# Performance work log

Hardware: AMD Instinct MI355X
Metric: run time of the kernel (lower is better)

Reference implementation:

```python
import jax, jax.numpy as jnp
import numpy as np

E = 128      # embedding_dim
H = 64       # hidden_dim
B = 2048     # batch
L = 200      # history length
NEG = -1e30  # stand-in for -inf (avoids NaN for all-pad rows; same math when any key unmasked)


def setup_inputs() -> dict:
    key = jax.random.key(0)
    ks = jax.random.split(key, 10)
    s1 = 1.0 / np.sqrt(4 * E)
    s2 = 1.0 / np.sqrt(H)
    return {
        "query": jax.random.normal(ks[0], (B, E), jnp.float32),
        "keys": jax.random.normal(ks[1], (B, L, E), jnp.float32),
        "mask": jax.random.randint(ks[2], (B, L), 0, 2, jnp.int32),
        "W1": jax.random.uniform(ks[3], (4 * E, H), jnp.float32, -s1, s1),
        "b1": jax.random.uniform(ks[4], (H,), jnp.float32, -s1, s1),
        "W2": jax.random.uniform(ks[5], (H, H), jnp.float32, -s2, s2),
        "b2": jax.random.uniform(ks[6], (H,), jnp.float32, -s2, s2),
        "W3": jax.random.uniform(ks[7], (H, 1), jnp.float32, -s2, s2),
        "b3": jax.random.uniform(ks[8], (1,), jnp.float32, -s2, s2),
        "no_hist": jax.random.normal(ks[9], (E,), jnp.float32) * 0.001,
    }


def reference(query, keys, mask, W1, b1, W2, b2, W3, b3, no_hist):
    # q expanded over L, 4-way concat features: [q, k, q*k, q-k] -> (B, L, 4E)
    q = jnp.broadcast_to(query[:, None, :], keys.shape)
    attn_in = jnp.concatenate([q, keys, q * keys, q - keys], axis=-1)
    # 3-layer MLP scorer -> (B, L)
    h = jax.nn.relu(attn_in @ W1 + b1)
    h = jax.nn.relu(h @ W2 + b2)
    scores = (h @ W3 + b3)[..., 0]
    # masked softmax over L, then zero masked slots and renormalize
    m = mask.astype(scores.dtype)
    scores = jnp.where(m == 0, NEG, scores)
    attn = jax.nn.softmax(scores, axis=1) * m
    denom = jnp.sum(attn, axis=1, keepdims=True)
    attn = attn / (denom + 1e-12)
    # weighted sum of keys -> (B, E)
    user_interest = jnp.einsum("bl,ble->be", attn, keys)
    # rows with no history get the learned no-hist embedding
    all_pad = jnp.sum(m, axis=1) == 0  # (B,)
    user_interest = jnp.where(all_pad[:, None], no_hist[None, :], user_interest)
    return user_interest
```

## Files before the change

### kernel.cpp

```cpp
#include <hip/hip_runtime.h>


#define NB 2048
#define LE 128
#define LH 64
#define LL 200

typedef short bf16x8 __attribute__((ext_vector_type(8)));
typedef float f32x4 __attribute__((ext_vector_type(4)));

__device__ float g_BD[8192];
__device__ float g_Cq[8192];
__device__ float g_AD[8192];
__device__ short g_W2T[4096];

__device__ __forceinline__ short f2bf(float f) {
  unsigned u = __float_as_uint(f);
  u += 0x7fffu + ((u >> 16) & 1u);
  return (short)(u >> 16);
}

__global__ void k0_prep(const float* __restrict__ W1, const float* __restrict__ W2) {
  int idx = blockIdx.x * 256 + threadIdx.x;
  if (idx < 8192) {
    int h = idx >> 7, e = idx & 127;
    g_BD[idx] = W1[(128 + e) * LH + h] - W1[(384 + e) * LH + h];
    g_Cq[idx] = W1[(256 + e) * LH + h];
    int e2 = idx >> 6, h2 = idx & 63;
    g_AD[idx] = W1[e2 * LH + h2] + W1[(384 + e2) * LH + h2];
    if (idx < 4096) {
      int c = idx >> 6, k = idx & 63;
      g_W2T[idx] = f2bf(W2[k * LH + c]);
    }
  }
}

struct __align__(16) SM {
  short flds1[16 * 64 * 8];
  short flds2[8 * 64 * 8];
  short h1[4][16 * 72];
  float scores[208];
  float q[128];
  float bias1[64];
  float b2s[64];
  float w3s[64];
  float red[16];
};

__global__ void __launch_bounds__(256, 4)
din_attn(const float* __restrict__ query, const float* __restrict__ keysg,
         const int* __restrict__ mask, const float* __restrict__ b1,
         const float* __restrict__ b2, const float* __restrict__ W3,
         const float* __restrict__ no_hist, float* __restrict__ out)
{
  __shared__ SM sm;
  const int b    = blockIdx.x;
  const int t    = threadIdx.x;
  const int lane = t & 63;
  const int wv   = t >> 6;
  const int col  = lane & 15;
  const int quad = lane >> 4;

  int my_mask = 0;
  if (t < LL) my_mask = mask[b * LL + t];
  if (t < LE) sm.q[t] = query[b * LE + t];
  if (t < LH) { sm.b2s[t] = b2[t]; sm.w3s[t] = W3[t]; }
  __syncthreads();

  #pragma unroll
  for (int i = 0; i < 4; ++i) {
    int idx = (t + 256 * i) * 8;
    int h = idx >> 7, e0 = idx & 127;
    float4 bd0 = *(const float4*)&g_BD[idx];
    float4 bd1 = *(const float4*)&g_BD[idx + 4];
    float4 c0  = *(const float4*)&g_Cq[idx];
    float4 c1  = *(const float4*)&g_Cq[idx + 4];
    bf16x8 w;
    w[0] = f2bf(bd0.x + sm.q[e0 + 0] * c0.x);
    w[1] = f2bf(bd0.y + sm.q[e0 + 1] * c0.y);
    w[2] = f2bf(bd0.z + sm.q[e0 + 2] * c0.z);
    w[3] = f2bf(bd0.w + sm.q[e0 + 3] * c0.w);
    w[4] = f2bf(bd1.x + sm.q[e0 + 4] * c1.x);
    w[5] = f2bf(bd1.y + sm.q[e0 + 5] * c1.y);
    w[6] = f2bf(bd1.z + sm.q[e0 + 6] * c1.z);
    w[7] = f2bf(bd1.w + sm.q[e0 + 7] * c1.w);
    int n = h >> 4, cc = h & 15, kt = e0 >> 5, qd = (e0 >> 3) & 3;
    *(bf16x8*)&sm.flds1[(((n * 4 + kt) * 64) + qd * 16 + cc) * 8] = w;
  }
  {
    int l = t & 63, f0 = t >> 6;
    #pragma unroll
    for (int ii = 0; ii < 2; ++ii) {
      int f = f0 + ii * 4;
      int n = f >> 1, k2 = f & 1;
      int cc = l & 15, qd = l >> 4;
      *(bf16x8*)&sm.flds2[(f * 64 + l) * 8] =
          *(const bf16x8*)&g_W2T[(n * 16 + cc) * 64 + k2 * 32 + qd * 8];
    }
  }
  {
    int h = lane;
    float acc = 0.f;
    #pragma unroll 8
    for (int e = wv * 32; e < wv * 32 + 32; ++e)
      acc = fmaf(sm.q[e], g_AD[e * LH + h], acc);
    float* biasp = (float*)&sm.h1[0][0];
    biasp[wv * 64 + h] = acc;
  }
  __syncthreads();

  if (t < LH) {
    const float* biasp = (const float*)&sm.h1[0][0];
    sm.bias1[t] = b1[t] + biasp[t] + biasp[64 + t] + biasp[128 + t] + biasp[192 + t];
  }
  __syncthreads();

  const float* kb = keysg + (size_t)b * LL * LE;
  short* h1w = &sm.h1[wv][0];
  const int mts[4] = {wv, wv + 4, wv + 8, 12};
  bf16x8 ka[4][4];

  auto load_tile = [&](bf16x8 (&a)[4], int mt) {
    int row = mt * 16 + col;
    row = row < LL ? row : LL - 1;
    const float* rp = kb + row * LE;
    #pragma unroll
    for (int kt = 0; kt < 4; ++kt) {
      float4 v0 = *(const float4*)&rp[kt * 32 + quad * 8];
      float4 v1 = *(const float4*)&rp[kt * 32 + quad * 8 + 4];
      bf16x8 av;
      av[0] = f2bf(v0.x); av[1] = f2bf(v0.y); av[2] = f2bf(v0.z); av[3] = f2bf(v0.w);
      av[4] = f2bf(v1.x); av[5] = f2bf(v1.y); av[6] = f2bf(v1.z); av[7] = f2bf(v1.w);
      a[kt] = av;
    }
  };

  auto compute_tile = [&](const bf16x8 (&a)[4], int mt) {
    #pragma unroll
    for (int n = 0; n < 4; ++n) {
      f32x4 acc = {0.f, 0.f, 0.f, 0.f};
      #pragma unroll
      for (int kt = 0; kt < 4; ++kt) {
        bf16x8 wf = *(const bf16x8*)&sm.flds1[((n * 4 + kt) * 64 + lane) * 8];
        acc = __builtin_amdgcn_mfma_f32_16x16x32_bf16(a[kt], wf, acc, 0, 0, 0);
      }
      float bias = sm.bias1[n * 16 + col];
      #pragma unroll
      for (int j = 0; j < 4; ++j)
        h1w[(quad * 4 + j) * 72 + n * 16 + col] = f2bf(fmaxf(acc[j] + bias, 0.f));
    }
    bf16x8 a2[2];
    #pragma unroll
    for (int k2 = 0; k2 < 2; ++k2)
      a2[k2] = *(const bf16x8*)&h1w[col * 72 + k2 * 32 + quad * 8];
    float p[4] = {0.f, 0.f, 0.f, 0.f};
    #pragma unroll
    for (int n = 0; n < 4; ++n) {
      bf16x8 w20 = *(const bf16x8*)&sm.flds2[((n * 2 + 0) * 64 + lane) * 8];
      bf16x8 w21 = *(const bf16x8*)&sm.flds2[((n * 2 + 1) * 64 + lane) * 8];
      f32x4 c2 = {0.f, 0.f, 0.f, 0.f};
      c2 = __builtin_amdgcn_mfma_f32_16x16x32_bf16(a2[0], w20, c2, 0, 0, 0);
      c2 = __builtin_amdgcn_mfma_f32_16x16x32_bf16(a2[1], w21, c2, 0, 0, 0);
      float bb = sm.b2s[n * 16 + col];
      float w3 = sm.w3s[n * 16 + col];
      #pragma unroll
      for (int j = 0; j < 4; ++j)
        p[j] = fmaf(fmaxf(c2[j] + bb, 0.f), w3, p[j]);
    }
    #pragma unroll
    for (int j = 0; j < 4; ++j) {
      #pragma unroll
      for (int off = 1; off < 16; off <<= 1)
        p[j] += __shfl_xor(p[j], off);
      if (col == 0) sm.scores[mt * 16 + quad * 4 + j] = p[j];
    }
  };

  load_tile(ka[0], mts[0]);
  load_tile(ka[1], mts[1]);
  compute_tile(ka[0], mts[0]);
  load_tile(ka[2], mts[2]);
  compute_tile(ka[1], mts[1]);
  if (wv == 0) load_tile(ka[3], 12);
  compute_tile(ka[2], mts[2]);
  if (wv == 0) compute_tile(ka[3], 12);
  __syncthreads();

  float sc = (t < LL) ? sm.scores[t] : -3.0e38f;
  float vmax = (my_mask != 0) ? sc : -3.0e38f;
  #pragma unroll
  for (int off = 1; off < 64; off <<= 1) vmax = fmaxf(vmax, __shfl_xor(vmax, off));
  if (lane == 0) sm.red[wv] = vmax;
  __syncthreads();
  float M = fmaxf(fmaxf(sm.red[0], sm.red[1]), fmaxf(sm.red[2], sm.red[3]));
  float ex = (t < LL && my_mask != 0) ? __expf(sc - M) : 0.f;
  float vsum = ex;
  #pragma unroll
  for (int off = 1; off < 64; off <<= 1) vsum += __shfl_xor(vsum, off);
  if (lane == 0) sm.red[4 + wv] = vsum;
  __syncthreads();
  float Z = sm.red[4] + sm.red[5] + sm.red[6] + sm.red[7];
  bool allpad = !(Z > 0.f);
  float rz = allpad ? 0.f : (1.f / Z);
  if (t < 208) sm.scores[t] = (t < LL) ? ex * rz : 0.f;
  __syncthreads();

  {
    const int nt = (wv == 0) ? 4 : 3;
    float aw[4] = {0.f, 0.f, 0.f, 0.f};
    #pragma unroll
    for (int i = 0; i < 4; ++i)
      if (i < nt) aw[i] = sm.scores[mts[i] * 16 + col];

    float* redf = (float*)&sm.h1[0][0];
    #pragma unroll
    for (int kt = 0; kt < 4; ++kt) {
      float s[8] = {0.f, 0.f, 0.f, 0.f, 0.f, 0.f, 0.f, 0.f};
      #pragma unroll
      for (int i = 0; i < 4; ++i) {
        if (i < nt) {
          const int* kv = (const int*)&ka[i][kt];
          #pragma unroll
          for (int w = 0; w < 4; ++w) {
            unsigned u = (unsigned)kv[w];
            s[2 * w]     = fmaf(aw[i], __uint_as_float(u << 16), s[2 * w]);
            s[2 * w + 1] = fmaf(aw[i], __uint_as_float(u & 0xffff0000u), s[2 * w + 1]);
          }
        }
      }
      #pragma unroll
      for (int j = 0; j < 8; ++j) {
        #pragma unroll
        for (int off = 1; off < 16; off <<= 1)
          s[j] += __shfl_xor(s[j], off);
      }
      if (col == 0) {
        #pragma unroll
        for (int j = 0; j < 8; ++j)
          redf[wv * 128 + kt * 32 + quad * 8 + j] = s[j];
      }
    }
    __syncthreads();
    if (t < LE) {
      float s = redf[t] + redf[128 + t] + redf[256 + t] + redf[384 + t];
      if (allpad) s = no_hist[t];
      out[b * LE + t] = s;
    }
  }
}

extern "C" void kernel_launch(void* const* d_in, const int* in_sizes, int n_in,
                              void* d_out, int out_size, void* d_ws, size_t ws_size,
                              hipStream_t stream) {
  (void)in_sizes; (void)n_in; (void)ws_size; (void)out_size; (void)d_ws;
  const float* query   = (const float*)d_in[0];
  const float* keysg   = (const float*)d_in[1];
  const int*   mask    = (const int*)d_in[2];
  const float* W1      = (const float*)d_in[3];
  const float* b1      = (const float*)d_in[4];
  const float* W2      = (const float*)d_in[5];
  const float* b2      = (const float*)d_in[6];
  const float* W3      = (const float*)d_in[7];
  const float* no_hist = (const float*)d_in[9];

  k0_prep<<<32, 256, 0, stream>>>(W1, W2);
  din_attn<<<NB, 256, 0, stream>>>(query, keysg, mask, b1, b2, W3, no_hist,
                                   (float*)d_out);
}
```

Measured before the change: 319.6 us.

## Use packed bf16 conversion, transposed MFMA output, and butterfly shuffle reductions

```diff
diff --git a/kernel.cpp b/kernel.cpp
--- a/kernel.cpp
+++ b/kernel.cpp
@@ -18,6 +18,12 @@
   unsigned u = __float_as_uint(f);
   u += 0x7fffu + ((u >> 16) & 1u);
   return (short)(u >> 16);
+}
+
+__device__ __forceinline__ unsigned cvtpk(float a, float b) {
+  unsigned d;
+  asm("v_cvt_pk_bf16_f32 %0, %1, %2" : "=v"(d) : "v"(a), "v"(b));
+  return d;
 }
 
 __global__ void k0_prep(const float* __restrict__ W1, const float* __restrict__ W2) {
@@ -38,13 +44,14 @@
 struct __align__(16) SM {
   short flds1[16 * 64 * 8];
   short flds2[8 * 64 * 8];
-  short h1[4][16 * 72];
+  short h1[4][16 * 68];
   float scores[208];
   float q[128];
   float bias1[64];
   float b2s[64];
   float w3s[64];
   float red[16];
+  float redf[512];
 };
 
 __global__ void __launch_bounds__(256, 4)
@@ -75,17 +82,13 @@
     float4 bd1 = *(const float4*)&g_BD[idx + 4];
     float4 c0  = *(const float4*)&g_Cq[idx];
     float4 c1  = *(const float4*)&g_Cq[idx + 4];
-    bf16x8 w;
-    w[0] = f2bf(bd0.x + sm.q[e0 + 0] * c0.x);
-    w[1] = f2bf(bd0.y + sm.q[e0 + 1] * c0.y);
-    w[2] = f2bf(bd0.z + sm.q[e0 + 2] * c0.z);
-    w[3] = f2bf(bd0.w + sm.q[e0 + 3] * c0.w);
-    w[4] = f2bf(bd1.x + sm.q[e0 + 4] * c1.x);
-    w[5] = f2bf(bd1.y + sm.q[e0 + 5] * c1.y);
-    w[6] = f2bf(bd1.z + sm.q[e0 + 6] * c1.z);
-    w[7] = f2bf(bd1.w + sm.q[e0 + 7] * c1.w);
+    int4 w;
+    w.x = (int)cvtpk(bd0.x + sm.q[e0 + 0] * c0.x, bd0.y + sm.q[e0 + 1] * c0.y);
+    w.y = (int)cvtpk(bd0.z + sm.q[e0 + 2] * c0.z, bd0.w + sm.q[e0 + 3] * c0.w);
+    w.z = (int)cvtpk(bd1.x + sm.q[e0 + 4] * c1.x, bd1.y + sm.q[e0 + 5] * c1.y);
+    w.w = (int)cvtpk(bd1.z + sm.q[e0 + 6] * c1.z, bd1.w + sm.q[e0 + 7] * c1.w);
     int n = h >> 4, cc = h & 15, kt = e0 >> 5, qd = (e0 >> 3) & 3;
-    *(bf16x8*)&sm.flds1[(((n * 4 + kt) * 64) + qd * 16 + cc) * 8] = w;
+    *(int4*)&sm.flds1[(((n * 4 + kt) * 64) + qd * 16 + cc) * 8] = w;
   }
   {
     int l = t & 63, f0 = t >> 6;
@@ -128,10 +131,12 @@
     for (int kt = 0; kt < 4; ++kt) {
       float4 v0 = *(const float4*)&rp[kt * 32 + quad * 8];
       float4 v1 = *(const float4*)&rp[kt * 32 + quad * 8 + 4];
-      bf16x8 av;
-      av[0] = f2bf(v0.x); av[1] = f2bf(v0.y); av[2] = f2bf(v0.z); av[3] = f2bf(v0.w);
-      av[4] = f2bf(v1.x); av[5] = f2bf(v1.y); av[6] = f2bf(v1.z); av[7] = f2bf(v1.w);
-      a[kt] = av;
+      int4 w;
+      w.x = (int)cvtpk(v0.x, v0.y);
+      w.y = (int)cvtpk(v0.z, v0.w);
+      w.z = (int)cvtpk(v1.x, v1.y);
+      w.w = (int)cvtpk(v1.z, v1.w);
+      a[kt] = *(bf16x8*)&w;
     }
   };
 
@@ -142,17 +147,18 @@
       #pragma unroll
       for (int kt = 0; kt < 4; ++kt) {
         bf16x8 wf = *(const bf16x8*)&sm.flds1[((n * 4 + kt) * 64 + lane) * 8];
-        acc = __builtin_amdgcn_mfma_f32_16x16x32_bf16(a[kt], wf, acc, 0, 0, 0);
+        acc = __builtin_amdgcn_mfma_f32_16x16x32_bf16(wf, a[kt], acc, 0, 0, 0);
       }
-      float bias = sm.bias1[n * 16 + col];
-      #pragma unroll
-      for (int j = 0; j < 4; ++j)
-        h1w[(quad * 4 + j) * 72 + n * 16 + col] = f2bf(fmaxf(acc[j] + bias, 0.f));
+      float4 bb = *(const float4*)&sm.bias1[n * 16 + quad * 4];
+      int2 wr;
+      wr.x = (int)cvtpk(fmaxf(acc[0] + bb.x, 0.f), fmaxf(acc[1] + bb.y, 0.f));
+      wr.y = (int)cvtpk(fmaxf(acc[2] + bb.z, 0.f), fmaxf(acc[3] + bb.w, 0.f));
+      *(int2*)&h1w[col * 68 + n * 16 + quad * 4] = wr;
     }
     bf16x8 a2[2];
     #pragma unroll
     for (int k2 = 0; k2 < 2; ++k2)
-      a2[k2] = *(const bf16x8*)&h1w[col * 72 + k2 * 32 + quad * 8];
+      a2[k2] = *(const bf16x8*)&h1w[col * 68 + k2 * 32 + quad * 8];
     float p[4] = {0.f, 0.f, 0.f, 0.f};
     #pragma unroll
     for (int n = 0; n < 4; ++n) {
@@ -167,12 +173,18 @@
       for (int j = 0; j < 4; ++j)
         p[j] = fmaf(fmaxf(c2[j] + bb, 0.f), w3, p[j]);
     }
-    #pragma unroll
-    for (int j = 0; j < 4; ++j) {
-      #pragma unroll
-      for (int off = 1; off < 16; off <<= 1)
-        p[j] += __shfl_xor(p[j], off);
-      if (col == 0) sm.scores[mt * 16 + quad * 4 + j] = p[j];
+    {
+      bool s8 = (col & 8) != 0;
+      float k0 = s8 ? p[2] : p[0], d0 = s8 ? p[0] : p[2];
+      float k1 = s8 ? p[3] : p[1], d1 = s8 ? p[1] : p[3];
+      k0 += __shfl_xor(d0, 8);
+      k1 += __shfl_xor(d1, 8);
+      bool s4 = (col & 4) != 0;
+      float u = s4 ? k1 : k0, du = s4 ? k0 : k1;
+      u += __shfl_xor(du, 4);
+      u += __shfl_xor(u, 2);
+      u += __shfl_xor(u, 1);
+      if ((col & 3) == 0) sm.scores[mt * 16 + quad * 4 + (col >> 2)] = u;
     }
   };
 
@@ -207,42 +219,44 @@
 
   {
     const int nt = (wv == 0) ? 4 : 3;
-    float aw[4] = {0.f, 0.f, 0.f, 0.f};
-    #pragma unroll
-    for (int i = 0; i < 4; ++i)
-      if (i < nt) aw[i] = sm.scores[mts[i] * 16 + col];
-
-    float* redf = (float*)&sm.h1[0][0];
-    #pragma unroll
-    for (int kt = 0; kt < 4; ++kt) {
-      float s[8] = {0.f, 0.f, 0.f, 0.f, 0.f, 0.f, 0.f, 0.f};
-      #pragma unroll
-      for (int i = 0; i < 4; ++i) {
-        if (i < nt) {
+    float v[32];
+    #pragma unroll
+    for (int k = 0; k < 32; ++k) v[k] = 0.f;
+    #pragma unroll
+    for (int i = 0; i < 4; ++i) {
+      if (i < nt) {
+        float aw = sm.scores[mts[i] * 16 + col];
+        #pragma unroll
+        for (int kt = 0; kt < 4; ++kt) {
           const int* kv = (const int*)&ka[i][kt];
           #pragma unroll
           for (int w = 0; w < 4; ++w) {
             unsigned u = (unsigned)kv[w];
-            s[2 * w]     = fmaf(aw[i], __uint_as_float(u << 16), s[2 * w]);
-            s[2 * w + 1] = fmaf(aw[i], __uint_as_float(u & 0xffff0000u), s[2 * w + 1]);
+            v[kt * 8 + 2 * w]     = fmaf(aw, __uint_as_float(u << 16), v[kt * 8 + 2 * w]);
+            v[kt * 8 + 2 * w + 1] = fmaf(aw, __uint_as_float(u & 0xffff0000u), v[kt * 8 + 2 * w + 1]);
           }
         }
       }
+    }
+    #pragma unroll
+    for (int step = 0; step < 4; ++step) {
+      const int off  = 8 >> step;
+      const int half = 16 >> step;
+      bool sel = (col & off) != 0;
       #pragma unroll
-      for (int j = 0; j < 8; ++j) {
-        #pragma unroll
-        for (int off = 1; off < 16; off <<= 1)
-          s[j] += __shfl_xor(s[j], off);
+      for (int k = 0; k < 16; ++k) {
+        if (k < half) {
+          float keep = sel ? v[k + half] : v[k];
+          float send = sel ? v[k] : v[k + half];
+          v[k] = keep + __shfl_xor(send, off);
+        }
       }
-      if (col == 0) {
-        #pragma unroll
-        for (int j = 0; j < 8; ++j)
-          redf[wv * 128 + kt * 32 + quad * 8 + j] = s[j];
-      }
-    }
+    }
+    int e0 = (col >> 2) * 32 + quad * 8 + ((col & 3) * 2);
+    *(float2*)&sm.redf[wv * 128 + e0] = make_float2(v[0], v[1]);
     __syncthreads();
     if (t < LE) {
-      float s = redf[t] + redf[128 + t] + redf[256 + t] + redf[384 + t];
+      float s = sm.redf[t] + sm.redf[128 + t] + sm.redf[256 + t] + sm.redf[384 + t];
       if (allpad) s = no_hist[t];
       out[b * LE + t] = s;
     }
```

Result: no change. 313.5 us (-1.9%).
